# Kernel tuning notes

Hardware: AMD Instinct MI355X
Metric: run time of the kernel (lower is better)

## Reference

```python
import jax, jax.numpy as jnp
import numpy as np

DIM = 1024
NUM_HEADS = 16
HEAD_DIM = DIM // NUM_HEADS
ROPE_BASE = 10000.0


def _rope_tables(seq_len, head_dim, dtype):
    # inv_freq over even indices, then freqs duplicated (cat(freqs, freqs))
    inv_freq = 1.0 / (ROPE_BASE ** (jnp.arange(0, head_dim, 2, dtype=jnp.float32) / head_dim))
    t = jnp.arange(seq_len, dtype=jnp.float32)
    freqs = jnp.einsum('i,j->ij', t, inv_freq)          # [N, head_dim/2]
    emb = jnp.concatenate([freqs, freqs], axis=-1)      # [N, head_dim]
    return jnp.cos(emb).astype(dtype), jnp.sin(emb).astype(dtype)


def _rotate_half(x):
    x1, x2 = jnp.split(x, 2, axis=-1)
    return jnp.concatenate([-x2, x1], axis=-1)


def setup_inputs() -> dict:
    key = jax.random.key(0)
    k1, k2, k3 = jax.random.split(key, 3)
    B, N = 2, 2048
    x = jax.random.normal(k1, (B, N, DIM), dtype=jnp.float32)
    w_qkv = jax.random.normal(k2, (3 * DIM, DIM), dtype=jnp.float32) * (DIM ** -0.5)
    w_out = jax.random.normal(k3, (DIM, DIM), dtype=jnp.float32) * (DIM ** -0.5)
    return {"x": x, "w_qkv": w_qkv, "w_out": w_out}


def reference(x, w_qkv, w_out):
    B, N, C = x.shape
    scale = HEAD_DIM ** -0.5
    qkv = x @ w_qkv.T                                   # [B, N, 3*C]
    qkv = qkv.reshape(B, N, 3, NUM_HEADS, HEAD_DIM)
    qkv = jnp.transpose(qkv, (2, 0, 3, 1, 4))           # [3, B, H, N, hd]
    q, k, v = qkv[0], qkv[1], qkv[2]

    cos, sin = _rope_tables(N, HEAD_DIM, x.dtype)       # [N, hd] each
    q = q * cos + _rotate_half(q) * sin
    k = k * cos + _rotate_half(k) * sin

    attn = jnp.einsum('bhqd,bhkd->bhqk', q, k) * scale  # [B, H, N, N]
    attn = jax.nn.softmax(attn, axis=-1)
    out = jnp.einsum('bhqk,bhkd->bhqd', attn, v)        # [B, H, N, hd]
    out = jnp.transpose(out, (0, 2, 1, 3)).reshape(B, N, C)
    return out @ w_out.T
```

## Files before the change

kernel.cpp:

```cpp
#include <hip/hip_runtime.h>
#include <stdint.h>


#define BATCH 2
#define SEQ   2048
#define DIM_C 1024
#define NHEAD 16
#define HD    64
#define MTOT  (BATCH * SEQ)
#define NQKV  (3 * DIM_C)
#define QSCALE 0.1803368801111204f

typedef _Float16 h8 __attribute__((ext_vector_type(8)));
typedef _Float16 h4v __attribute__((ext_vector_type(4)));
typedef float    f4 __attribute__((ext_vector_type(4)));
typedef unsigned int u4v __attribute__((ext_vector_type(4)));

#if __has_builtin(__builtin_amdgcn_exp2f)
#define EXP2(x) __builtin_amdgcn_exp2f(x)
#else
#define EXP2(x) exp2f(x)
#endif

__device__ __forceinline__ f4 mfma16(h8 a, h8 b, f4 c) {
  return __builtin_amdgcn_mfma_f32_16x16x32_f16(a, b, c, 0, 0, 0);
}

__device__ __forceinline__ unsigned pk2(float a, float b) {
  auto t = __builtin_amdgcn_cvt_pkrtz(a, b);
  unsigned u;
  __builtin_memcpy(&u, &t, 4);
  return u;
}

__device__ __forceinline__ void swap32(unsigned& a, unsigned& b) {
#if __has_builtin(__builtin_amdgcn_permlane32_swap)
  typedef unsigned u2_ __attribute__((ext_vector_type(2)));
  u2_ r = __builtin_amdgcn_permlane32_swap(a, b, false, false);
  a = r[0]; b = r[1];
#else
  const bool hi = (threadIdx.x & 32) != 0;
  unsigned sa = __shfl_xor(a, 32), sb = __shfl_xor(b, 32);
  unsigned na = hi ? sb : a, nb = hi ? b : sa;
  a = na; b = nb;
#endif
}
__device__ __forceinline__ void swap16(unsigned& a, unsigned& b) {
#if __has_builtin(__builtin_amdgcn_permlane16_swap)
  typedef unsigned u2_ __attribute__((ext_vector_type(2)));
  u2_ r = __builtin_amdgcn_permlane16_swap(a, b, false, false);
  a = r[0]; b = r[1];
#else
  const bool hi = (threadIdx.x & 16) != 0;
  unsigned sa = __shfl_xor(a, 16), sb = __shfl_xor(b, 16);
  unsigned na = hi ? sb : a, nb = hi ? b : sa;
  a = na; b = nb;
#endif
}

__device__ __forceinline__ void gload16(const _Float16* g, _Float16* l) {
  __builtin_amdgcn_global_load_lds(
      (const __attribute__((address_space(1))) void*)g,
      (__attribute__((address_space(3))) void*)l, 16, 0, 0);
}

#define N4X  1048576
#define N4WQ 786432
#define N4WO 262144
#define CVT_TOT (N4X + N4WQ + N4WO)
__global__ void prep_kernel(const float* __restrict__ x,
                            const float* __restrict__ wq,
                            const float* __restrict__ wo,
                            _Float16* __restrict__ xh,
                            _Float16* __restrict__ wqh,
                            _Float16* __restrict__ woh,
                            float* __restrict__ cosT, float* __restrict__ sinT) {
  int idx = blockIdx.x * blockDim.x + threadIdx.x;
  if (idx < CVT_TOT) {
    const float* s; _Float16* d; int i;
    if (idx < N4X) { s = x; d = xh; i = idx; }
    else if (idx < N4X + N4WQ) { s = wq; d = wqh; i = idx - N4X; }
    else { s = wo; d = woh; i = idx - (N4X + N4WQ); }
    float4 v = reinterpret_cast<const float4*>(s)[i];
    h4v o = {(_Float16)v.x, (_Float16)v.y, (_Float16)v.z, (_Float16)v.w};
    reinterpret_cast<h4v*>(d)[i] = o;
  } else {
    int t = idx - CVT_TOT;
    int n = t >> 5, j = t & 31;
    float inv = powf(10000.0f, -(float)(2 * j) / 64.0f);
    float a = (float)n * inv;
    cosT[t] = cosf(a);
    sinT[t] = sinf(a);
  }
}

__global__ __launch_bounds__(256) void gemm_qkv(const _Float16* __restrict__ A,
                                                const _Float16* __restrict__ Bm,
                                                const float* __restrict__ cosT,
                                                const float* __restrict__ sinT,
                                                _Float16* __restrict__ qh,
                                                _Float16* __restrict__ kh,
                                                _Float16* __restrict__ vh) {
  const int K = DIM_C;
  __shared__ _Float16 Ah[2][64 * 64];
  __shared__ _Float16 Bh[2][64 * 64];
  const int tid = threadIdx.x;
  const int wave = tid >> 6, lane = tid & 63;
  const int lr = lane & 15, lg = lane >> 4;
  const int p = blockIdx.x;
  const int wg = (p & 7) * 96 + (p >> 3);
  const int bx = wg >> 5, by = wg & 31;
  const int m0 = by * 128, n0 = bx * 128;
  const int wr = (wave >> 1) * 64, wc = (wave & 1) * 64;

  const f4 zf = {0.f, 0.f, 0.f, 0.f};
  f4 acc[4][4];
#pragma unroll
  for (int i = 0; i < 4; ++i)
#pragma unroll
    for (int j = 0; j < 4; ++j) acc[i][j] = zf;

  const _Float16* Ab = A + (size_t)m0 * K;
  const _Float16* Bb = Bm + (size_t)n0 * K;

  auto stage = [&](int ks, int bi) {
#pragma unroll
    for (int it = 0; it < 2; ++it) {
      int c = tid + it * 256;
      int lrow = c >> 3;
      int sch = (c & 7) ^ (lrow & 7);
      int mrow = lrow * 2 + (sch >> 2), part = sch & 3;
      gload16(Ab + (size_t)mrow * K + ks * 32 + part * 8, &Ah[bi][c * 8]);
      gload16(Bb + (size_t)mrow * K + ks * 32 + part * 8, &Bh[bi][c * 8]);
    }
  };

  const int rch = (((lr & 1) * 4 + lg) ^ (lr >> 1)) * 8;
  const int lrb = lr >> 1;

  stage(0, 0);
  const int ksteps = K >> 5;
  for (int ks = 0; ks < ksteps; ++ks) {
    __syncthreads();
    int cur = ks & 1;
    if (ks + 1 < ksteps) stage(ks + 1, cur ^ 1);

    h8 af[4], bf[4];
#pragma unroll
    for (int i = 0; i < 4; ++i)
      af[i] = *(const h8*)&Ah[cur][(wr / 2 + i * 8 + lrb) * 64 + rch];
#pragma unroll
    for (int j = 0; j < 4; ++j)
      bf[j] = *(const h8*)&Bh[cur][(wc / 2 + j * 8 + lrb) * 64 + rch];
#pragma unroll
    for (int i = 0; i < 4; ++i)
#pragma unroll
      for (int j = 0; j < 4; ++j) acc[i][j] = mfma16(af[i], bf[j], acc[i][j]);
  }

  const int nc = n0 + wc;
  const int s = nc >> 10;
  const int hcol = (nc >> 6) & 15;
  _Float16* dst = (s == 0) ? qh : (s == 1) ? kh : vh;
  const float scl = (s == 0) ? QSCALE : 1.0f;
#pragma unroll
  for (int i = 0; i < 4; ++i)
#pragma unroll
    for (int r = 0; r < 4; ++r) {
      int row = m0 + wr + i * 16 + lg * 4 + r;
      int n = row & (SEQ - 1);
      _Float16* drow = dst + ((size_t)(((row >> 11) * NHEAD + hcol) * SEQ + n)) * HD;
      h4v o;
      if (s == 2) {
        o = {(_Float16)acc[i][0][r], (_Float16)acc[i][1][r],
             (_Float16)acc[i][2][r], (_Float16)acc[i][3][r]};
      } else {
        float c0 = cosT[n * 32 + lr],      sn0 = sinT[n * 32 + lr];
        float c1 = cosT[n * 32 + 16 + lr], sn1 = sinT[n * 32 + 16 + lr];
        float a10 = acc[i][0][r], a20 = acc[i][2][r];
        float a11 = acc[i][1][r], a21 = acc[i][3][r];
        o = {(_Float16)((a10 * c0 - a20 * sn0) * scl),
             (_Float16)((a11 * c1 - a21 * sn1) * scl),
             (_Float16)((a20 * c0 + a10 * sn0) * scl),
             (_Float16)((a21 * c1 + a11 * sn1) * scl)};
      }
      *(h4v*)&drow[lr * 4] = o;
    }
}

__global__ __launch_bounds__(256) void gemm_out(const _Float16* __restrict__ A,
                                                const _Float16* __restrict__ Bm,
                                                float* __restrict__ Cv) {
  const int K = DIM_C, N = DIM_C;
  __shared__ _Float16 Ah[2][64 * 64];
  __shared__ _Float16 Bh[2][32 * 64];
  const int tid = threadIdx.x;
  const int wave = tid >> 6, lane = tid & 63;
  const int lr = lane & 15, lg = lane >> 4;
  const int p = blockIdx.x;
  const int wg = (p & 7) * 64 + (p >> 3);
  const int bx = wg >> 5, by = wg & 31;
  const int m0 = by * 128, n0 = bx * 64;
  const int wr = (wave >> 1) * 64, wc = (wave & 1) * 32;

  const f4 zf = {0.f, 0.f, 0.f, 0.f};
  f4 acc[4][2];
#pragma unroll
  for (int i = 0; i < 4; ++i)
#pragma unroll
    for (int j = 0; j < 2; ++j) acc[i][j] = zf;

  const _Float16* Ab = A + (size_t)m0 * K;
  const _Float16* Bb = Bm + (size_t)n0 * K;

  auto stage = [&](int ks, int bi) {
#pragma unroll
    for (int it = 0; it < 2; ++it) {
      int c = tid + it * 256;
      int lrow = c >> 3;
      int sch = (c & 7) ^ (lrow & 7);
      int mrow = lrow * 2 + (sch >> 2), part = sch & 3;
      gload16(Ab + (size_t)mrow * K + ks * 32 + part * 8, &Ah[bi][c * 8]);
    }
    int c = tid;
    int lrow = c >> 3;
    int sch = (c & 7) ^ (lrow & 7);
    int mrow = lrow * 2 + (sch >> 2), part = sch & 3;
    gload16(Bb + (size_t)mrow * K + ks * 32 + part * 8, &Bh[bi][c * 8]);
  };

  const int rch = (((lr & 1) * 4 + lg) ^ (lr >> 1)) * 8;
  const int lrb = lr >> 1;

  stage(0, 0);
  const int ksteps = K >> 5;
  for (int ks = 0; ks < ksteps; ++ks) {
    __syncthreads();
    int cur = ks & 1;
    if (ks + 1 < ksteps) stage(ks + 1, cur ^ 1);

    h8 af[4], bf[2];
#pragma unroll
    for (int i = 0; i < 4; ++i)
      af[i] = *(const h8*)&Ah[cur][(wr / 2 + i * 8 + lrb) * 64 + rch];
#pragma unroll
    for (int j = 0; j < 2; ++j)
      bf[j] = *(const h8*)&Bh[cur][(wc / 2 + j * 8 + lrb) * 64 + rch];
#pragma unroll
    for (int i = 0; i < 4; ++i)
#pragma unroll
      for (int j = 0; j < 2; ++j) acc[i][j] = mfma16(af[i], bf[j], acc[i][j]);
  }

#pragma unroll
  for (int i = 0; i < 4; ++i)
#pragma unroll
    for (int j = 0; j < 2; ++j)
#pragma unroll
      for (int r = 0; r < 4; ++r) {
        size_t row = (size_t)(m0 + wr + i * 16 + lg * 4 + r);
        int col = n0 + wc + j * 16 + lr;
        Cv[row * N + col] = acc[i][j][r];
      }
}

__global__ void vtrans_kernel(const _Float16* __restrict__ v, _Float16* __restrict__ vt) {
  int blk = blockIdx.x;
  int bh = blk >> 6, nt = blk & 63;
  int d = threadIdx.x & 63, w = threadIdx.x >> 6;
  int pp = (d & 15) * 4 + (d >> 4);
  int n0 = nt * 32 + w * 8;
  const _Float16* src = v + (size_t)bh * SEQ * HD;
  _Float16* dst = vt + ((size_t)bh * HD + d) * SEQ;
  h8 o;
#pragma unroll
  for (int j = 0; j < 8; ++j) o[j] = src[(size_t)(n0 + j) * HD + pp];
  *(h8*)(dst + n0) = o;
}

__global__ __launch_bounds__(256, 2) void attn_kernel(const _Float16* __restrict__ qh,
                                                      const _Float16* __restrict__ kh,
                                                      const _Float16* __restrict__ vt,
                                                      _Float16* __restrict__ aoh) {
  __shared__ _Float16 Kt[2][128 * 64];
  __shared__ _Float16 Vt[2][64 * 128];

  const int tid = threadIdx.x, wave = tid >> 6, lane = tid & 63;
  const int lr = lane & 15, lg = lane >> 4;
  const int p = blockIdx.x;
  const int wg = (p & 7) * 64 + (p >> 3);
  const int bh = wg >> 4;
  const int qt = wg & 15;
  const int b = bh >> 4, h = bh & 15;

  const _Float16* Qb = qh + (size_t)bh * SEQ * HD;
  const _Float16* Kb = kh + (size_t)bh * SEQ * HD;
  const _Float16* Vb = vt + (size_t)bh * HD * SEQ;
  const int q0 = qt * 128 + wave * 32;

  int kOf[2], vOf[2][2];
#pragma unroll
  for (int cc = 0; cc < 2; ++cc) kOf[cc] = ((cc * 4 + lg) ^ (lr & 7)) * 8;
#pragma unroll
  for (int sub = 0; sub < 2; ++sub)
#pragma unroll
    for (int cc = 0; cc < 2; ++cc) vOf[sub][cc] = ((sub * 8 + cc * 4 + lg) ^ lr) * 8;

  h8 aq[2][2];
#pragma unroll
  for (int r2 = 0; r2 < 2; ++r2)
#pragma unroll
    for (int c = 0; c < 2; ++c)
      aq[r2][c] = *(const h8*)(Qb + (size_t)(q0 + r2 * 16 + lr) * HD + c * 32 + lg * 8);

  const h8 onesv = {(_Float16)1.f, (_Float16)1.f, (_Float16)1.f, (_Float16)1.f,
                    (_Float16)1.f, (_Float16)1.f, (_Float16)1.f, (_Float16)1.f};
  const f4 zf = {0.f, 0.f, 0.f, 0.f};
  f4 lacc[2] = {zf, zf};
  f4 acc[2][4];
#pragma unroll
  for (int r2 = 0; r2 < 2; ++r2)
#pragma unroll
    for (int dt = 0; dt < 4; ++dt) acc[r2][dt] = zf;

  auto stage = [&](int kt, int bi) {
    const _Float16* Ks = Kb + (size_t)kt * 128 * HD;
    const _Float16* Vs = Vb + kt * 128;
#pragma unroll
    for (int it = 0; it < 4; ++it) {
      int c = tid + it * 256;
      int krow = c >> 3, kpart = c & 7;
      int ksp = kpart ^ (krow & 7);
      gload16(Ks + (size_t)krow * HD + ksp * 8, &Kt[bi][c * 8]);
      int vrow = c >> 4, vpart = c & 15;
      int vsp = vpart ^ (vrow & 15);
      gload16(Vs + (size_t)vrow * SEQ + vsp * 8, &Vt[bi][c * 8]);
    }
  };

  stage(0, 0);
  for (int t = 0; t < SEQ / 128; ++t) {
    __syncthreads();
    const int cur = t & 1;
    if (t + 1 < SEQ / 128) stage(t + 1, cur ^ 1);

    const _Float16* Kbuf = &Kt[cur][0];
    const _Float16* Vbuf = &Vt[cur][0];
#pragma unroll
    for (int sub = 0; sub < 2; ++sub) {
      h8 bk[4][2], vb[4][2];
      const _Float16* Krow = Kbuf + (sub * 64 + lr) * 64;
#pragma unroll
      for (int ct = 0; ct < 4; ++ct)
#pragma unroll
        for (int cc = 0; cc < 2; ++cc)
          bk[ct][cc] = *(const h8*)(Krow + ct * 16 * 64 + kOf[cc]);
      const _Float16* Vrow = Vbuf + lr * 128;
#pragma unroll
      for (int dt = 0; dt < 4; ++dt)
#pragma unroll
        for (int cc = 0; cc < 2; ++cc)
          vb[dt][cc] = *(const h8*)(Vrow + dt * 16 * 128 + vOf[sub][cc]);

#pragma unroll
      for (int r2 = 0; r2 < 2; ++r2) {
        f4 St[4];
        __builtin_amdgcn_s_setprio(1);
#pragma unroll
        for (int ct = 0; ct < 4; ++ct) {
          f4 z = mfma16(bk[ct][0], aq[r2][0], zf);
          St[ct] = mfma16(bk[ct][1], aq[r2][1], z);
        }
        __builtin_amdgcn_s_setprio(0);

        unsigned w[4][2];
#pragma unroll
        for (int ct = 0; ct < 4; ++ct) {
          w[ct][0] = pk2(EXP2(St[ct][0]), EXP2(St[ct][1]));
          w[ct][1] = pk2(EXP2(St[ct][2]), EXP2(St[ct][3]));
        }
        swap32(w[0][0], w[1][0]); swap32(w[0][1], w[1][1]);
        swap32(w[2][0], w[3][0]); swap32(w[2][1], w[3][1]);
        swap16(w[0][0], w[1][0]); swap16(w[0][1], w[1][1]);
        swap16(w[2][0], w[3][0]); swap16(w[2][1], w[3][1]);
        u4v pw0 = {w[0][0], w[0][1], w[1][0], w[1][1]};
        u4v pw1 = {w[2][0], w[2][1], w[3][0], w[3][1]};
        h8 pa0, pa1;
        __builtin_memcpy(&pa0, &pw0, 16);
        __builtin_memcpy(&pa1, &pw1, 16);

        __builtin_amdgcn_s_setprio(1);
        lacc[r2] = mfma16(onesv, pa0, lacc[r2]);
        lacc[r2] = mfma16(onesv, pa1, lacc[r2]);
#pragma unroll
        for (int dt = 0; dt < 4; ++dt) {
          acc[r2][dt] = mfma16(vb[dt][0], pa0, acc[r2][dt]);
          acc[r2][dt] = mfma16(vb[dt][1], pa1, acc[r2][dt]);
        }
        __builtin_amdgcn_s_setprio(0);
      }
    }
  }

#pragma unroll
  for (int r2 = 0; r2 < 2; ++r2) {
    float inv = 1.0f / lacc[r2][0];
    int q = q0 + r2 * 16 + lr;
#pragma unroll
    for (int dt = 0; dt < 4; ++dt) {
      h4v o = {(_Float16)(acc[r2][dt][0] * inv), (_Float16)(acc[r2][dt][1] * inv),
               (_Float16)(acc[r2][dt][2] * inv), (_Float16)(acc[r2][dt][3] * inv)};
      *(h4v*)&aoh[((size_t)(b * SEQ + q)) * DIM_C + h * HD + dt * 16 + lg * 4] = o;
    }
  }
}

extern "C" void kernel_launch(void* const* d_in, const int* in_sizes, int n_in,
                              void* d_out, int out_size, void* d_ws, size_t ws_size,
                              hipStream_t stream) {
  const float* x     = (const float*)d_in[0];
  const float* w_qkv = (const float*)d_in[1];
  const float* w_out = (const float*)d_in[2];
  float* out = (float*)d_out;

  char* w = (char*)d_ws;
  _Float16* xh    = (_Float16*)(w + 0);
  _Float16* wqkvh = (_Float16*)(w + 8388608);
  _Float16* wouth = (_Float16*)(w + 14680064);
  _Float16* qhp   = (_Float16*)(w + 16777216);
  _Float16* khp   = (_Float16*)(w + 25165824);
  _Float16* vhp   = (_Float16*)(w + 33554432);
  _Float16* vtp   = (_Float16*)(w + 41943040);
  _Float16* aohp  = (_Float16*)(w + 50331648);
  float*    cosT  = (float*)(w + 58720256);
  float*    sinT  = (float*)(w + 58982400);

  prep_kernel<<<(CVT_TOT + SEQ * 32) / 256, 256, 0, stream>>>(
      x, w_qkv, w_out, xh, wqkvh, wouth, cosT, sinT);

  gemm_qkv<<<768, 256, 0, stream>>>(xh, wqkvh, cosT, sinT, qhp, khp, vhp);

  vtrans_kernel<<<32 * 64, 256, 0, stream>>>(vhp, vtp);

  attn_kernel<<<32 * 16, 256, 0, stream>>>(qhp, khp, vtp, aohp);

  gemm_out<<<512, 256, 0, stream>>>(aohp, wouth, out);
}
```

Measured before the change: 129.3 us.

## Split attention waves across query and KV halves with LDS reduction

The four waves of an attention block become two query groups of 64 rows times two KV halves, instead of four waves of 32 query rows each sweeping the whole KV tile. Each K/V fragment read from LDS is now reused across four query subtiles instead of two, which cuts LDS read traffic per MFMA. The two KV halves' partial accumulators and row sums are combined through shared memory in an epilogue. In exchange, per-wave register pressure goes up (more accumulators and score tiles live at once), and an extra synchronised reduction is added; the 65-float row stride also makes the 16-byte LDS stores misaligned.

```diff
diff --git a/kernel.cpp b/kernel.cpp
--- a/kernel.cpp
+++ b/kernel.cpp
@@ -282,11 +282,13 @@
                                                       const _Float16* __restrict__ kh,
                                                       const _Float16* __restrict__ vt,
                                                       _Float16* __restrict__ aoh) {
-  __shared__ _Float16 Kt[2][128 * 64];
-  __shared__ _Float16 Vt[2][64 * 128];
+  __shared__ __align__(16) char smem[65536];
+  _Float16* KtB = (_Float16*)smem;
+  _Float16* VtB = (_Float16*)(smem + 32768);
 
   const int tid = threadIdx.x, wave = tid >> 6, lane = tid & 63;
   const int lr = lane & 15, lg = lane >> 4;
+  const int qw = wave >> 1, kvw = wave & 1;
   const int p = blockIdx.x;
   const int wg = (p & 7) * 64 + (p >> 3);
   const int bh = wg >> 4;
@@ -296,19 +298,18 @@
   const _Float16* Qb = qh + (size_t)bh * SEQ * HD;
   const _Float16* Kb = kh + (size_t)bh * SEQ * HD;
   const _Float16* Vb = vt + (size_t)bh * HD * SEQ;
-  const int q0 = qt * 128 + wave * 32;
-
-  int kOf[2], vOf[2][2];
-#pragma unroll
-  for (int cc = 0; cc < 2; ++cc) kOf[cc] = ((cc * 4 + lg) ^ (lr & 7)) * 8;
-#pragma unroll
-  for (int sub = 0; sub < 2; ++sub)
-#pragma unroll
-    for (int cc = 0; cc < 2; ++cc) vOf[sub][cc] = ((sub * 8 + cc * 4 + lg) ^ lr) * 8;
-
-  h8 aq[2][2];
-#pragma unroll
-  for (int r2 = 0; r2 < 2; ++r2)
+  const int q0 = qt * 128 + qw * 64;
+
+  int kOf[2], vOf[2];
+#pragma unroll
+  for (int cc = 0; cc < 2; ++cc) {
+    kOf[cc] = ((cc * 4 + lg) ^ (lr & 7)) * 8;
+    vOf[cc] = ((kvw * 8 + cc * 4 + lg) ^ lr) * 8;
+  }
+
+  h8 aq[4][2];
+#pragma unroll
+  for (int r2 = 0; r2 < 4; ++r2)
 #pragma unroll
     for (int c = 0; c < 2; ++c)
       aq[r2][c] = *(const h8*)(Qb + (size_t)(q0 + r2 * 16 + lr) * HD + c * 32 + lg * 8);
@@ -316,25 +317,27 @@
   const h8 onesv = {(_Float16)1.f, (_Float16)1.f, (_Float16)1.f, (_Float16)1.f,
                     (_Float16)1.f, (_Float16)1.f, (_Float16)1.f, (_Float16)1.f};
   const f4 zf = {0.f, 0.f, 0.f, 0.f};
-  f4 lacc[2] = {zf, zf};
-  f4 acc[2][4];
-#pragma unroll
-  for (int r2 = 0; r2 < 2; ++r2)
+  f4 lacc[4] = {zf, zf, zf, zf};
+  f4 acc[4][4];
+#pragma unroll
+  for (int r2 = 0; r2 < 4; ++r2)
 #pragma unroll
     for (int dt = 0; dt < 4; ++dt) acc[r2][dt] = zf;
 
   auto stage = [&](int kt, int bi) {
     const _Float16* Ks = Kb + (size_t)kt * 128 * HD;
     const _Float16* Vs = Vb + kt * 128;
+    _Float16* kb = KtB + bi * 8192;
+    _Float16* vb = VtB + bi * 8192;
 #pragma unroll
     for (int it = 0; it < 4; ++it) {
       int c = tid + it * 256;
       int krow = c >> 3, kpart = c & 7;
       int ksp = kpart ^ (krow & 7);
-      gload16(Ks + (size_t)krow * HD + ksp * 8, &Kt[bi][c * 8]);
+      gload16(Ks + (size_t)krow * HD + ksp * 8, kb + c * 8);
       int vrow = c >> 4, vpart = c & 15;
       int vsp = vpart ^ (vrow & 15);
-      gload16(Vs + (size_t)vrow * SEQ + vsp * 8, &Vt[bi][c * 8]);
+      gload16(Vs + (size_t)vrow * SEQ + vsp * 8, vb + c * 8);
     }
   };
 
@@ -344,73 +347,93 @@
     const int cur = t & 1;
     if (t + 1 < SEQ / 128) stage(t + 1, cur ^ 1);
 
-    const _Float16* Kbuf = &Kt[cur][0];
-    const _Float16* Vbuf = &Vt[cur][0];
-#pragma unroll
-    for (int sub = 0; sub < 2; ++sub) {
-      h8 bk[4][2], vb[4][2];
-      const _Float16* Krow = Kbuf + (sub * 64 + lr) * 64;
-#pragma unroll
-      for (int ct = 0; ct < 4; ++ct)
-#pragma unroll
-        for (int cc = 0; cc < 2; ++cc)
-          bk[ct][cc] = *(const h8*)(Krow + ct * 16 * 64 + kOf[cc]);
-      const _Float16* Vrow = Vbuf + lr * 128;
+    h8 kf[4][2];
+    const _Float16* Krow = KtB + cur * 8192 + (kvw * 64 + lr) * 64;
+#pragma unroll
+    for (int ct = 0; ct < 4; ++ct)
+#pragma unroll
+      for (int cc = 0; cc < 2; ++cc)
+        kf[ct][cc] = *(const h8*)(Krow + ct * 16 * 64 + kOf[cc]);
+
+    f4 St[4][4];
+    __builtin_amdgcn_s_setprio(1);
+#pragma unroll
+    for (int r2 = 0; r2 < 4; ++r2)
+#pragma unroll
+      for (int ct = 0; ct < 4; ++ct) {
+        f4 z = mfma16(kf[ct][0], aq[r2][0], zf);
+        St[r2][ct] = mfma16(kf[ct][1], aq[r2][1], z);
+      }
+    __builtin_amdgcn_s_setprio(0);
+
+    h8 vf[4][2];
+    const _Float16* Vrow = VtB + cur * 8192 + lr * 128;
+#pragma unroll
+    for (int dt = 0; dt < 4; ++dt)
+#pragma unroll
+      for (int cc = 0; cc < 2; ++cc)
+        vf[dt][cc] = *(const h8*)(Vrow + dt * 16 * 128 + vOf[cc]);
+
+#pragma unroll
+    for (int r2 = 0; r2 < 4; ++r2) {
+      unsigned w[4][2];
+#pragma unroll
+      for (int ct = 0; ct < 4; ++ct) {
+        w[ct][0] = pk2(EXP2(St[r2][ct][0]), EXP2(St[r2][ct][1]));
+        w[ct][1] = pk2(EXP2(St[r2][ct][2]), EXP2(St[r2][ct][3]));
+      }
+      swap32(w[0][0], w[1][0]); swap32(w[0][1], w[1][1]);
+      swap32(w[2][0], w[3][0]); swap32(w[2][1], w[3][1]);
+      swap16(w[0][0], w[1][0]); swap16(w[0][1], w[1][1]);
+      swap16(w[2][0], w[3][0]); swap16(w[2][1], w[3][1]);
+      u4v pw0 = {w[0][0], w[0][1], w[1][0], w[1][1]};
+      u4v pw1 = {w[2][0], w[2][1], w[3][0], w[3][1]};
+      h8 pa0, pa1;
+      __builtin_memcpy(&pa0, &pw0, 16);
+      __builtin_memcpy(&pa1, &pw1, 16);
+
+      __builtin_amdgcn_s_setprio(1);
+      lacc[r2] = mfma16(onesv, pa0, lacc[r2]);
+      lacc[r2] = mfma16(onesv, pa1, lacc[r2]);
+#pragma unroll
+      for (int dt = 0; dt < 4; ++dt) {
+        acc[r2][dt] = mfma16(vf[dt][0], pa0, acc[r2][dt]);
+        acc[r2][dt] = mfma16(vf[dt][1], pa1, acc[r2][dt]);
+      }
+      __builtin_amdgcn_s_setprio(0);
+    }
+  }
+
+  __syncthreads();
+  float* pl = (float*)smem;
+  float* lp = (float*)(smem + 34816);
+
+  if (kvw == 1) {
+#pragma unroll
+    for (int r2 = 0; r2 < 4; ++r2) {
+      int ql = qw * 64 + r2 * 16 + lr;
 #pragma unroll
       for (int dt = 0; dt < 4; ++dt)
-#pragma unroll
-        for (int cc = 0; cc < 2; ++cc)
-          vb[dt][cc] = *(const h8*)(Vrow + dt * 16 * 128 + vOf[sub][cc]);
-
-#pragma unroll
-      for (int r2 = 0; r2 < 2; ++r2) {
-        f4 St[4];
-        __builtin_amdgcn_s_setprio(1);
-#pragma unroll
-        for (int ct = 0; ct < 4; ++ct) {
-          f4 z = mfma16(bk[ct][0], aq[r2][0], zf);
-          St[ct] = mfma16(bk[ct][1], aq[r2][1], z);
-        }
-        __builtin_amdgcn_s_setprio(0);
-
-        unsigned w[4][2];
-#pragma unroll
-        for (int ct = 0; ct < 4; ++ct) {
-          w[ct][0] = pk2(EXP2(St[ct][0]), EXP2(St[ct][1]));
-          w[ct][1] = pk2(EXP2(St[ct][2]), EXP2(St[ct][3]));
-        }
-        swap32(w[0][0], w[1][0]); swap32(w[0][1], w[1][1]);
-        swap32(w[2][0], w[3][0]); swap32(w[2][1], w[3][1]);
-        swap16(w[0][0], w[1][0]); swap16(w[0][1], w[1][1]);
-        swap16(w[2][0], w[3][0]); swap16(w[2][1], w[3][1]);
-        u4v pw0 = {w[0][0], w[0][1], w[1][0], w[1][1]};
-        u4v pw1 = {w[2][0], w[2][1], w[3][0], w[3][1]};
-        h8 pa0, pa1;
-        __builtin_memcpy(&pa0, &pw0, 16);
-        __builtin_memcpy(&pa1, &pw1, 16);
-
-        __builtin_amdgcn_s_setprio(1);
-        lacc[r2] = mfma16(onesv, pa0, lacc[r2]);
-        lacc[r2] = mfma16(onesv, pa1, lacc[r2]);
-#pragma unroll
-        for (int dt = 0; dt < 4; ++dt) {
-          acc[r2][dt] = mfma16(vb[dt][0], pa0, acc[r2][dt]);
-          acc[r2][dt] = mfma16(vb[dt][1], pa1, acc[r2][dt]);
-        }
-        __builtin_amdgcn_s_setprio(0);
-      }
-    }
-  }
-
-#pragma unroll
-  for (int r2 = 0; r2 < 2; ++r2) {
-    float inv = 1.0f / lacc[r2][0];
-    int q = q0 + r2 * 16 + lr;
-#pragma unroll
-    for (int dt = 0; dt < 4; ++dt) {
-      h4v o = {(_Float16)(acc[r2][dt][0] * inv), (_Float16)(acc[r2][dt][1] * inv),
-               (_Float16)(acc[r2][dt][2] * inv), (_Float16)(acc[r2][dt][3] * inv)};
-      *(h4v*)&aoh[((size_t)(b * SEQ + q)) * DIM_C + h * HD + dt * 16 + lg * 4] = o;
+        *(f4*)&pl[(size_t)ql * 65 + dt * 16 + lg * 4] = acc[r2][dt];
+      if (lg == 0) lp[ql] = lacc[r2][0];
+    }
+  }
+  __syncthreads();
+  if (kvw == 0) {
+#pragma unroll
+    for (int r2 = 0; r2 < 4; ++r2) {
+      int ql = qw * 64 + r2 * 16 + lr;
+      float lt = lacc[r2][0] + lp[ql];
+      float inv = 1.0f / lt;
+      int q = q0 + r2 * 16 + lr;
+#pragma unroll
+      for (int dt = 0; dt < 4; ++dt) {
+        f4 oth = *(const f4*)&pl[(size_t)ql * 65 + dt * 16 + lg * 4];
+        f4 s = acc[r2][dt] + oth;
+        h4v o = {(_Float16)(s[0] * inv), (_Float16)(s[1] * inv),
+                 (_Float16)(s[2] * inv), (_Float16)(s[3] * inv)};
+        *(h4v*)&aoh[((size_t)(b * SEQ + q)) * DIM_C + h * HD + dt * 16 + lg * 4] = o;
+      }
     }
   }
 }
```

After: 128.6 us (median of 2 runs). No clear change (-0.5%).
